# Performance work log

Hardware: AMD Instinct MI355X
Metric: run time of the kernel (lower is better)

The kernel has to match this reference:

```python
import jax, jax.numpy as jnp
import numpy as np

L, H, C, HS, V, BS = 4, 8, 512, 64, 32000, 2048  # layers, heads, n_embd, head_size, vocab, block_size
B, T = 2, 2048


def _ln(x, g, b, eps=1e-5):
    m = jnp.mean(x, axis=-1, keepdims=True)
    v = jnp.var(x, axis=-1, keepdims=True)
    return (x - m) * jax.lax.rsqrt(v + eps) * g + b


def setup_inputs() -> dict:
    key = jax.random.key(0)
    ks = jax.random.split(key, 12)
    s = 0.02
    f = jnp.float32
    return {
        "idx": jax.random.randint(ks[0], (B, T), 0, V),
        "tok_emb": jax.random.normal(ks[1], (V, C), f) * s,
        "pos_emb": jax.random.normal(ks[2], (BS, C), f) * s,
        "ln1_g": jnp.ones((L, C), f), "ln1_b": jnp.zeros((L, C), f),
        "wq": jax.random.normal(ks[3], (L, H, C, HS), f) * s,
        "wk": jax.random.normal(ks[4], (L, H, C, HS), f) * s,
        "wv": jax.random.normal(ks[5], (L, H, C, HS), f) * s,
        "proj_w": jax.random.normal(ks[6], (L, C, C), f) * s,
        "proj_b": jnp.zeros((L, C), f),
        "ln2_g": jnp.ones((L, C), f), "ln2_b": jnp.zeros((L, C), f),
        "ff_w1": jax.random.normal(ks[7], (L, C, 4 * C), f) * s,
        "ff_b1": jnp.zeros((L, 4 * C), f),
        "ff_w2": jax.random.normal(ks[8], (L, 4 * C, C), f) * s,
        "ff_b2": jnp.zeros((L, C), f),
        "ffln_g": jnp.ones((L, C), f), "ffln_b": jnp.zeros((L, C), f),
        "lm_w": jax.random.normal(ks[9], (C, V), f) * s,
        "lm_b": jnp.zeros((V,), f),
    }


def reference(idx, tok_emb, pos_emb, ln1_g, ln1_b, wq, wk, wv, proj_w, proj_b,
              ln2_g, ln2_b, ff_w1, ff_b1, ff_w2, ff_b2, ffln_g, ffln_b, lm_w, lm_b):
    Tn = idx.shape[1]
    x = tok_emb[idx] + pos_emb[:Tn]  # [B,T,C]
    causal = jnp.tril(jnp.ones((Tn, Tn), bool))
    for l in range(L):
        h = _ln(x, ln1_g[l], ln1_b[l])
        q = jnp.einsum('btc,hcd->bhtd', h, wq[l])
        k = jnp.einsum('btc,hcd->bhtd', h, wk[l])
        v = jnp.einsum('btc,hcd->bhtd', h, wv[l])
        # NOTE: original module does NOT scale by 1/sqrt(head_size)
        wei = jnp.einsum('bhtd,bhsd->bhts', q, k)
        wei = jnp.where(causal, wei, -jnp.inf)
        wei = jax.nn.softmax(wei, axis=-1)
        att = jnp.einsum('bhts,bhsd->bhtd', wei, v)  # [B,H,T,HS]
        att = att.transpose(0, 2, 1, 3).reshape(x.shape[0], Tn, C)
        x = x + att @ proj_w[l].T + proj_b[l]
        h2 = _ln(x, ln2_g[l], ln2_b[l])
        ff = jax.nn.relu(h2 @ ff_w1[l] + ff_b1[l]) @ ff_w2[l] + ff_b2[l]
        ff = _ln(ff, ffln_g[l], ffln_b[l])  # FeedForward has trailing LayerNorm
        x = x + ff
    logits = x @ lm_w + lm_b  # [B,T,V]
    return logits
```

## Files before the change

kernel.cpp:

```cpp
#include <hip/hip_runtime.h>
#include <math.h>

#define NLAYER 4
#define NH     8
#define CDIM   512
#define HS     64
#define VOCAB  32000
#define BB     2
#define TT     2048
#define MROWS  (BB*TT)
#define QKVW   (3*CDIM)
#define NHEADS (BB*NH)
#define ASPLIT 4

typedef __attribute__((ext_vector_type(8))) short bf16x8;
typedef __attribute__((ext_vector_type(4))) float f32x4;

__device__ __forceinline__ unsigned short f2bf(float f) {
    unsigned int u = __float_as_uint(f);
    u += 0x7FFF + ((u >> 16) & 1);
    return (unsigned short)(u >> 16);
}

#define GLOAD16(g, l) __builtin_amdgcn_global_load_lds( \
    (const __attribute__((address_space(1))) void*)(g), \
    (__attribute__((address_space(3))) void*)(l), 16, 0, 0)

#define SWZ(row, chunk) (((row)*64) + ((((chunk) ^ ((row)&7)))*8))

template<int FLAGS, bool OUTBF, bool MSWIZ>
__global__ __launch_bounds__(256) void mfma_gemm(
    const unsigned short* __restrict__ A, int lda,
    const unsigned short* __restrict__ Bt, int ldb,
    const float* __restrict__ bias,
    void* __restrict__ Cout, int ldc,
    const float* __restrict__ resid,
    int K)
{
    __shared__ unsigned short As[2][128*64];
    __shared__ unsigned short Bs[2][128*64];
    const int tid = threadIdx.x;
    const int w = tid >> 6, l = tid & 63;
    const int wr = w >> 1, wc = w & 1;
    long m0, n0;
    if (MSWIZ) {
        const int mt = gridDim.x;
        const int flat = blockIdx.y * mt + blockIdx.x;
        const int cpx = (mt * gridDim.y) >> 3;
        const int swz = (flat & 7) * cpx + (flat >> 3);
        m0 = (long)(swz % mt) * 128;
        n0 = (long)(swz / mt) * 128;
    } else {
        m0 = (long)blockIdx.y * 128;
        n0 = (long)blockIdx.x * 128;
    }
    const int srow = l >> 3;
    const int scol = ((l & 7) ^ (srow & 7)) << 3;
    const unsigned short* Ab = A + m0*lda;
    const unsigned short* Bb = Bt + n0*ldb;
    const int fr = l & 15;
    const int g  = l >> 4;

    f32x4 acc[4][4];
    #pragma unroll
    for (int m = 0; m < 4; m++)
        #pragma unroll
        for (int n = 0; n < 4; n++) acc[m][n] = (f32x4)0.0f;

    auto stage = [&](int k0, int buf) {
        #pragma unroll
        for (int i = 0; i < 4; i++) {
            int seg = w*4 + i;
            GLOAD16(Ab + (long)(seg*8 + srow)*lda + k0 + scol, &As[buf][seg*512]);
            GLOAD16(Bb + (long)(seg*8 + srow)*ldb + k0 + scol, &Bs[buf][seg*512]);
        }
    };

    const int nk = K >> 6;
    stage(0, 0);
    for (int ks = 0; ks < nk; ks++) {
        const int buf = ks & 1;
        __syncthreads();
        if (ks + 1 < nk) stage((ks+1) << 6, buf ^ 1);
        #pragma unroll
        for (int kk = 0; kk < 2; kk++) {
            bf16x8 af[4], bf[4];
            #pragma unroll
            for (int m = 0; m < 4; m++) {
                int row = wr*64 + m*16 + fr;
                af[m] = *(const bf16x8*)&As[buf][SWZ(row, kk*4 + g)];
            }
            #pragma unroll
            for (int n = 0; n < 4; n++) {
                int row = wc*64 + n*16 + fr;
                bf[n] = *(const bf16x8*)&Bs[buf][SWZ(row, kk*4 + g)];
            }
            #pragma unroll
            for (int m = 0; m < 4; m++)
                #pragma unroll
                for (int n = 0; n < 4; n++)
                    acc[m][n] = __builtin_amdgcn_mfma_f32_16x16x32_bf16(
                        af[m], bf[n], acc[m][n], 0, 0, 0);
        }
    }

    const int rg = g << 2;
    #pragma unroll
    for (int n = 0; n < 4; n++) {
        long gn = n0 + wc*64 + n*16 + fr;
        float bv = (FLAGS & 1) ? bias[gn] : 0.f;
        #pragma unroll
        for (int m = 0; m < 4; m++) {
            #pragma unroll
            for (int r = 0; r < 4; r++) {
                long gm = m0 + wr*64 + m*16 + rg + r;
                float val = acc[m][n][r] + bv;
                if (FLAGS & 2) val = fmaxf(val, 0.f);
                if (FLAGS & 4) val += resid[gm*ldc + gn];
                if (OUTBF) {
                    ((unsigned short*)Cout)[gm*ldc + gn] = f2bf(val);
                } else if (FLAGS & 8) {
                    __builtin_nontemporal_store(val, &((float*)Cout)[gm*ldc + gn]);
                } else {
                    ((float*)Cout)[gm*ldc + gn] = val;
                }
            }
        }
    }
}

__global__ __launch_bounds__(256) void mfma_gemm_qkv(
    const unsigned short* __restrict__ A,
    const unsigned short* __restrict__ Bt,
    unsigned short* __restrict__ qh,
    unsigned short* __restrict__ kh,
    unsigned short* __restrict__ vt)
{
    __shared__ unsigned short As[2][128*64];
    __shared__ unsigned short Bs[2][128*64];
    const int tid = threadIdx.x;
    const int w = tid >> 6, l = tid & 63;
    const int wr = w >> 1, wc = w & 1;
    const long m0 = (long)blockIdx.y * 128;
    const long n0 = (long)blockIdx.x * 128;
    const int srow = l >> 3;
    const int scol = ((l & 7) ^ (srow & 7)) << 3;
    const unsigned short* Ab = A + m0*CDIM;
    const unsigned short* Bb = Bt + n0*CDIM;
    const int fr = l & 15;
    const int g  = l >> 4;

    f32x4 acc[4][4];
    #pragma unroll
    for (int m = 0; m < 4; m++)
        #pragma unroll
        for (int n = 0; n < 4; n++) acc[m][n] = (f32x4)0.0f;

    auto stage = [&](int k0, int buf) {
        #pragma unroll
        for (int i = 0; i < 4; i++) {
            int seg = w*4 + i;
            GLOAD16(Ab + (long)(seg*8 + srow)*CDIM + k0 + scol, &As[buf][seg*512]);
            GLOAD16(Bb + (long)(seg*8 + srow)*CDIM + k0 + scol, &Bs[buf][seg*512]);
        }
    };

    const int nk = CDIM >> 6;
    stage(0, 0);
    for (int ks = 0; ks < nk; ks++) {
        const int buf = ks & 1;
        __syncthreads();
        if (ks + 1 < nk) stage((ks+1) << 6, buf ^ 1);
        #pragma unroll
        for (int kk = 0; kk < 2; kk++) {
            bf16x8 af[4], bf[4];
            #pragma unroll
            for (int m = 0; m < 4; m++) {
                int row = wr*64 + m*16 + fr;
                af[m] = *(const bf16x8*)&As[buf][SWZ(row, kk*4 + g)];
            }
            #pragma unroll
            for (int n = 0; n < 4; n++) {
                int row = wc*64 + n*16 + fr;
                bf[n] = *(const bf16x8*)&Bs[buf][SWZ(row, kk*4 + g)];
            }
            #pragma unroll
            for (int m = 0; m < 4; m++)
                #pragma unroll
                for (int n = 0; n < 4; n++)
                    acc[m][n] = __builtin_amdgcn_mfma_f32_16x16x32_bf16(
                        af[m], bf[n], acc[m][n], 0, 0, 0);
        }
    }

    const int rg = g << 2;
    #pragma unroll
    for (int n = 0; n < 4; n++) {
        int gn = (int)(n0 + wc*64 + n*16 + fr);
        int which = gn >> 9, hh = (gn >> 6) & 7, d = gn & 63;
        #pragma unroll
        for (int m = 0; m < 4; m++) {
            #pragma unroll
            for (int r = 0; r < 4; r++) {
                int gm = (int)(m0 + wr*64 + m*16 + rg + r);
                int b = gm >> 11, t = gm & (TT-1);
                int head = b*NH + hh;
                unsigned short val = f2bf(acc[m][n][r]);
                if (which == 0)      qh[((long)head*TT + t)*HS + d] = val;
                else if (which == 1) kh[((long)head*TT + t)*HS + d] = val;
                else                 vt[((long)head*HS + d)*TT + t] = val;
            }
        }
    }
}

__global__ __launch_bounds__(256) void attn_part(
    const unsigned short* __restrict__ qh,
    const unsigned short* __restrict__ kh,
    const unsigned short* __restrict__ vt,
    float* __restrict__ oP, float* __restrict__ ml)
{
    __shared__ unsigned short Ks[2][64*64];
    __shared__ unsigned short Vts[2][64*64];
    __shared__ unsigned short Ps[4][32*72];
    const int tid = threadIdx.x;
    const int w = tid >> 6, l = tid & 63;
    const int fr = l & 15, g = l >> 4;
    const int head = blockIdx.y;
    const int sp = blockIdx.z;
    const int x = blockIdx.x;
    const int qw = x*128 + w*32;
    const unsigned short* Qb = qh + (long)head*TT*HS;
    const unsigned short* Kb = kh + (long)head*TT*HS;
    const unsigned short* Vb = vt + (long)head*HS*TT;

    bf16x8 aq[2][2];
    #pragma unroll
    for (int mt = 0; mt < 2; mt++)
        #pragma unroll
        for (int ks = 0; ks < 2; ks++)
            aq[mt][ks] = *(const bf16x8*)&Qb[(long)(qw + mt*16 + fr)*HS + ks*32 + g*8];

    f32x4 acc_o[2][4];
    float mrun[2][4], lsum[2][4];
    #pragma unroll
    for (int mt = 0; mt < 2; mt++) {
        #pragma unroll
        for (int r = 0; r < 4; r++) { mrun[mt][r] = -INFINITY; lsum[mt][r] = 0.f; }
        #pragma unroll
        for (int n = 0; n < 4; n++) acc_o[mt][n] = (f32x4)0.0f;
    }

    const int nch = 2*x + 2;
    const int qq = nch >> 2, rr = nch & 3;
    const int cbeg = sp*qq + (sp < rr ? sp : rr);
    const int cend = cbeg + qq + (sp < rr ? 1 : 0);
    const int srow = l >> 3;
    const int scol = ((l & 7) ^ (srow & 7)) << 3;

    auto stage = [&](int c) {
        int buf = c & 1;
        int s0_ = c*64;
        #pragma unroll
        for (int i = 0; i < 2; i++) {
            int rb = i*32 + w*8;
            GLOAD16(Kb + (long)(s0_ + rb + srow)*HS + scol, &Ks[buf][rb*64]);
            GLOAD16(Vb + (long)(rb + srow)*TT + s0_ + scol, &Vts[buf][rb*64]);
        }
    };

    if (cbeg < cend) stage(cbeg);
    for (int c = cbeg; c < cend; c++) {
        const int s0 = c*64;
        const int buf = c & 1;
        __syncthreads();
        if (c + 1 < cend) stage(c+1);
        if (s0 > qw + 31) continue;

        bf16x8 bk[4][2];
        #pragma unroll
        for (int n = 0; n < 4; n++)
            #pragma unroll
            for (int ks = 0; ks < 2; ks++) {
                int row = n*16 + fr;
                bk[n][ks] = *(const bf16x8*)&Ks[buf][SWZ(row, ks*4 + g)];
            }
        f32x4 sc[2][4];
        #pragma unroll
        for (int mt = 0; mt < 2; mt++)
            #pragma unroll
            for (int n = 0; n < 4; n++) sc[mt][n] = (f32x4)0.0f;
        #pragma unroll
        for (int ks = 0; ks < 2; ks++)
            #pragma unroll
            for (int mt = 0; mt < 2; mt++)
                #pragma unroll
                for (int n = 0; n < 4; n++)
                    sc[mt][n] = __builtin_amdgcn_mfma_f32_16x16x32_bf16(
                        aq[mt][ks], bk[n][ks], sc[mt][n], 0, 0, 0);

        #pragma unroll
        for (int mt = 0; mt < 2; mt++) {
            #pragma unroll
            for (int r = 0; r < 4; r++) {
                int q = qw + mt*16 + g*4 + r;
                float rmax = -INFINITY;
                #pragma unroll
                for (int n = 0; n < 4; n++) {
                    float v = sc[mt][n][r];
                    v = (s0 + n*16 + fr <= q) ? v : -INFINITY;
                    sc[mt][n][r] = v;
                    rmax = fmaxf(rmax, v);
                }
                #pragma unroll
                for (int off = 8; off >= 1; off >>= 1)
                    rmax = fmaxf(rmax, __shfl_xor(rmax, off));
                float mnew = fmaxf(mrun[mt][r], rmax);
                float scale = __expf(mrun[mt][r] - mnew);
                float ps = 0.f;
                #pragma unroll
                for (int n = 0; n < 4; n++) {
                    float p = __expf(sc[mt][n][r] - mnew);
                    sc[mt][n][r] = p;
                    ps += p;
                }
                #pragma unroll
                for (int off = 8; off >= 1; off >>= 1)
                    ps += __shfl_xor(ps, off);
                lsum[mt][r] = lsum[mt][r]*scale + ps;
                mrun[mt][r] = mnew;
                #pragma unroll
                for (int n = 0; n < 4; n++) acc_o[mt][n][r] *= scale;
            }
        }

        #pragma unroll
        for (int mt = 0; mt < 2; mt++)
            #pragma unroll
            for (int n = 0; n < 4; n++)
                #pragma unroll
                for (int r = 0; r < 4; r++)
                    Ps[w][(mt*16 + g*4 + r)*72 + n*16 + fr] = f2bf(sc[mt][n][r]);

        bf16x8 ap[2][2], bv[4][2];
        #pragma unroll
        for (int mt = 0; mt < 2; mt++)
            #pragma unroll
            for (int ks = 0; ks < 2; ks++)
                ap[mt][ks] = *(const bf16x8*)&Ps[w][(mt*16 + fr)*72 + ks*32 + g*8];
        #pragma unroll
        for (int n = 0; n < 4; n++)
            #pragma unroll
            for (int ks = 0; ks < 2; ks++) {
                int row = n*16 + fr;
                bv[n][ks] = *(const bf16x8*)&Vts[buf][SWZ(row, ks*4 + g)];
            }
        #pragma unroll
        for (int ks = 0; ks < 2; ks++)
            #pragma unroll
            for (int mt = 0; mt < 2; mt++)
                #pragma unroll
                for (int n = 0; n < 4; n++)
                    acc_o[mt][n] = __builtin_amdgcn_mfma_f32_16x16x32_bf16(
                        ap[mt][ks], bv[n][ks], acc_o[mt][n], 0, 0, 0);
    }

    float* oB = oP + ((long)(head*ASPLIT + sp)*TT)*HS;
    float* mlB = ml + ((long)(head*ASPLIT + sp)*TT)*2;
    #pragma unroll
    for (int mt = 0; mt < 2; mt++) {
        #pragma unroll
        for (int n = 0; n < 4; n++)
            #pragma unroll
            for (int r = 0; r < 4; r++)
                oB[(long)(qw + mt*16 + g*4 + r)*HS + n*16 + fr] = acc_o[mt][n][r];
        if (fr == 0) {
            #pragma unroll
            for (int r = 0; r < 4; r++) {
                int t = qw + mt*16 + g*4 + r;
                mlB[t*2]     = mrun[mt][r];
                mlB[t*2 + 1] = lsum[mt][r];
            }
        }
    }
}

__global__ __launch_bounds__(256) void attn_combine(
    const float* __restrict__ oP, const float* __restrict__ ml,
    unsigned short* __restrict__ att)
{
    const int gid = blockIdx.x*4 + (threadIdx.x >> 6);
    const int lane = threadIdx.x & 63;
    const int head = gid >> 11, t = gid & (TT-1);
    const int b = head >> 3, hh = head & 7;
    float m[ASPLIT], lv[ASPLIT];
    float M = -INFINITY;
    #pragma unroll
    for (int s = 0; s < ASPLIT; s++) {
        long i = (long)(head*ASPLIT + s)*TT + t;
        m[s] = ml[i*2]; lv[s] = ml[i*2+1];
        M = fmaxf(M, m[s]);
    }
    float L = 0.f, v = 0.f;
    #pragma unroll
    for (int s = 0; s < ASPLIT; s++) {
        float e = __expf(m[s] - M);
        L += lv[s]*e;
        v += oP[((long)(head*ASPLIT + s)*TT + t)*HS + lane]*e;
    }
    att[((long)b*TT + t)*CDIM + hh*HS + lane] = f2bf(v / L);
}

__global__ __launch_bounds__(256) void transpose_cast(
    const float* __restrict__ in, unsigned short* __restrict__ out,
    int R, int Cn, long in_z1, long in_z2, long out_z1, long out_z2, int z2n)
{
    const int z = blockIdx.z;
    const int z1 = z / z2n, z2 = z % z2n;
    const float* ip = in + (long)z1*in_z1 + (long)z2*in_z2;
    unsigned short* op = out + (long)z1*out_z1 + (long)z2*out_z2;
    __shared__ float tile[32][33];
    const int tx = threadIdx.x & 31, ty = threadIdx.x >> 5;
    const long r0 = (long)blockIdx.y*32, c0 = (long)blockIdx.x*32;
    #pragma unroll
    for (int i = 0; i < 4; i++)
        tile[ty + i*8][tx] = ip[(r0 + ty + i*8)*Cn + c0 + tx];
    __syncthreads();
    #pragma unroll
    for (int i = 0; i < 4; i++)
        op[(c0 + ty + i*8)*R + r0 + tx] = f2bf(tile[tx][ty + i*8]);
}

__global__ __launch_bounds__(256) void cast_kernel(
    const float* __restrict__ in, unsigned short* __restrict__ out, long n)
{
    long i = ((long)blockIdx.x*256 + threadIdx.x) * 4;
    if (i >= n) return;
    float4 v = *(const float4*)(in + i);
    ushort4 u = make_ushort4(f2bf(v.x), f2bf(v.y), f2bf(v.z), f2bf(v.w));
    *(ushort4*)(out + i) = u;
}

__global__ void embed_kernel(const int* __restrict__ idx,
                             const float* __restrict__ tok,
                             const float* __restrict__ pos,
                             float* __restrict__ x)
{
    const int r = blockIdx.x;
    const int t = r & (TT-1);
    const long tr = idx[r];
    const float* te = tok + tr*CDIM;
    const float* pe = pos + (long)t*CDIM;
    float* xo = x + (long)r*CDIM;
    for (int c = threadIdx.x; c < CDIM; c += blockDim.x)
        xo[c] = te[c] + pe[c];
}

template<int MODE>
__global__ __launch_bounds__(256) void ln_kernel(
    const float* __restrict__ in, const float* __restrict__ g,
    const float* __restrict__ bb, void* __restrict__ outp,
    void* __restrict__ outp2)
{
    const int wave = threadIdx.x >> 6;
    const int lane = threadIdx.x & 63;
    const long r = (long)blockIdx.x*4 + wave;
    const float* xr = in + r*CDIM;
    float vals[8];
    float s = 0.f;
    #pragma unroll
    for (int i = 0; i < 8; i++) { vals[i] = xr[lane + i*64]; s += vals[i]; }
    #pragma unroll
    for (int o = 32; o >= 1; o >>= 1) s += __shfl_xor(s, o);
    const float mean = s * (1.f/CDIM);
    float vs = 0.f;
    #pragma unroll
    for (int i = 0; i < 8; i++) { float d = vals[i]-mean; vs += d*d; }
    #pragma unroll
    for (int o = 32; o >= 1; o >>= 1) vs += __shfl_xor(vs, o);
    const float rstd = rsqrtf(vs*(1.f/CDIM) + 1e-5f);
    #pragma unroll
    for (int i = 0; i < 8; i++) {
        int c = lane + i*64;
        float nv = (vals[i]-mean)*rstd*g[c] + bb[c];
        if (MODE == 1) {
            ((unsigned short*)outp)[r*CDIM + c] = f2bf(nv);
        } else {
            float s2 = ((float*)outp)[r*CDIM + c] + nv;
            ((float*)outp)[r*CDIM + c] = s2;
            if (MODE == 3) ((unsigned short*)outp2)[r*CDIM + c] = f2bf(s2);
        }
    }
}

extern "C" void kernel_launch(void* const* d_in, const int* in_sizes, int n_in,
                              void* d_out, int out_size, void* d_ws, size_t ws_size,
                              hipStream_t stream)
{
    const int*   idx   = (const int*)  d_in[0];
    const float* tok   = (const float*)d_in[1];
    const float* pos   = (const float*)d_in[2];
    const float* ln1g  = (const float*)d_in[3];
    const float* ln1b  = (const float*)d_in[4];
    const float* wq    = (const float*)d_in[5];
    const float* wk    = (const float*)d_in[6];
    const float* wv    = (const float*)d_in[7];
    const float* projw = (const float*)d_in[8];
    const float* projb = (const float*)d_in[9];
    const float* ln2g  = (const float*)d_in[10];
    const float* ln2b  = (const float*)d_in[11];
    const float* ffw1  = (const float*)d_in[12];
    const float* ffb1  = (const float*)d_in[13];
    const float* ffw2  = (const float*)d_in[14];
    const float* ffb2  = (const float*)d_in[15];
    const float* flng  = (const float*)d_in[16];
    const float* flnb  = (const float*)d_in[17];
    const float* lmw   = (const float*)d_in[18];
    const float* lmb   = (const float*)d_in[19];
    float* out = (float*)d_out;

    char* wp = (char*)d_ws;
    float* x  = (float*)wp;           wp += (size_t)MROWS*CDIM*4;
    float* ff = (float*)wp;           wp += (size_t)MROWS*CDIM*4;
    unsigned short* h     = (unsigned short*)wp; wp += (size_t)MROWS*CDIM*2;
    unsigned short* lmt   = (unsigned short*)wp; wp += (size_t)VOCAB*CDIM*2;
    unsigned short* ff1t  = (unsigned short*)wp; wp += (size_t)NLAYER*4*CDIM*CDIM*2;
    unsigned short* ff2t  = (unsigned short*)wp; wp += (size_t)NLAYER*4*CDIM*CDIM*2;
    unsigned short* qkvt  = (unsigned short*)wp; wp += (size_t)NLAYER*QKVW*CDIM*2;
    unsigned short* projc = (unsigned short*)wp; wp += (size_t)NLAYER*CDIM*CDIM*2;
    unsigned short* qh    = (unsigned short*)wp; wp += (size_t)NHEADS*TT*HS*2;
    unsigned short* kh    = (unsigned short*)wp; wp += (size_t)NHEADS*TT*HS*2;
    unsigned short* vt    = (unsigned short*)wp; wp += (size_t)NHEADS*TT*HS*2;

    unsigned short* f1  = (unsigned short*)d_out;
    unsigned short* att = f1 + (size_t)MROWS*4*CDIM;
    float* oP = (float*)(att + (size_t)MROWS*CDIM);
    float* ml = oP + (size_t)NHEADS*ASPLIT*TT*HS;

    transpose_cast<<<dim3(VOCAB/32, CDIM/32, 1), 256, 0, stream>>>(
        lmw, lmt, CDIM, VOCAB, 0, 0, 0, 0, 1);
    transpose_cast<<<dim3(4*CDIM/32, CDIM/32, NLAYER), 256, 0, stream>>>(
        ffw1, ff1t, CDIM, 4*CDIM, (long)CDIM*4*CDIM, 0, (long)4*CDIM*CDIM, 0, 1);
    transpose_cast<<<dim3(CDIM/32, 4*CDIM/32, NLAYER), 256, 0, stream>>>(
        ffw2, ff2t, 4*CDIM, CDIM, (long)4*CDIM*CDIM, 0, (long)CDIM*4*CDIM, 0, 1);
    {
        const size_t QBLK = (size_t)CDIM * CDIM;
        transpose_cast<<<dim3(HS/32, CDIM/32, NLAYER*NH), 256, 0, stream>>>(
            wq, qkvt,            CDIM, HS,
            (long)NH*CDIM*HS, (long)CDIM*HS, (long)QKVW*CDIM, (long)HS*CDIM, NH);
        transpose_cast<<<dim3(HS/32, CDIM/32, NLAYER*NH), 256, 0, stream>>>(
            wk, qkvt + QBLK,     CDIM, HS,
            (long)NH*CDIM*HS, (long)CDIM*HS, (long)QKVW*CDIM, (long)HS*CDIM, NH);
        transpose_cast<<<dim3(HS/32, CDIM/32, NLAYER*NH), 256, 0, stream>>>(
            wv, qkvt + 2*QBLK,   CDIM, HS,
            (long)NH*CDIM*HS, (long)CDIM*HS, (long)QKVW*CDIM, (long)HS*CDIM, NH);
    }
    cast_kernel<<<(NLAYER*CDIM*CDIM/4 + 255)/256, 256, 0, stream>>>(
        projw, projc, (long)NLAYER*CDIM*CDIM);

    embed_kernel<<<MROWS, 256, 0, stream>>>(idx, tok, pos, x);

    for (int l = 0; l < NLAYER; l++) {
        const unsigned short* qkvt_l = qkvt + (size_t)l*QKVW*CDIM;
        const unsigned short* projc_l = projc + (size_t)l*CDIM*CDIM;
        const unsigned short* ff1t_l = ff1t + (size_t)l*4*CDIM*CDIM;
        const unsigned short* ff2t_l = ff2t + (size_t)l*4*CDIM*CDIM;

        ln_kernel<1><<<MROWS/4, 256, 0, stream>>>(x, ln1g + l*CDIM, ln1b + l*CDIM, h, nullptr);

        mfma_gemm_qkv<<<dim3(QKVW/128, MROWS/128), 256, 0, stream>>>(
            h, qkvt_l, qh, kh, vt);

        attn_part<<<dim3(TT/128, NHEADS, ASPLIT), 256, 0, stream>>>(qh, kh, vt, oP, ml);
        attn_combine<<<dim3(NHEADS*TT/4), 256, 0, stream>>>(oP, ml, att);

        mfma_gemm<5,false,false><<<dim3(CDIM/128, MROWS/128), 256, 0, stream>>>(
            att, CDIM, projc_l, CDIM, projb + l*CDIM, x, CDIM, x, CDIM);

        ln_kernel<1><<<MROWS/4, 256, 0, stream>>>(x, ln2g + l*CDIM, ln2b + l*CDIM, h, nullptr);

        mfma_gemm<3,true,false><<<dim3(4*CDIM/128, MROWS/128), 256, 0, stream>>>(
            h, CDIM, ff1t_l, CDIM, ffb1 + (size_t)l*4*CDIM, f1, 4*CDIM, nullptr, CDIM);

        mfma_gemm<1,false,false><<<dim3(CDIM/128, MROWS/128), 256, 0, stream>>>(
            f1, 4*CDIM, ff2t_l, 4*CDIM, ffb2 + l*CDIM, ff, CDIM, nullptr, 4*CDIM);

        if (l == NLAYER-1)
            ln_kernel<3><<<MROWS/4, 256, 0, stream>>>(ff, flng + l*CDIM, flnb + l*CDIM, x, h);
        else
            ln_kernel<2><<<MROWS/4, 256, 0, stream>>>(ff, flng + l*CDIM, flnb + l*CDIM, x, nullptr);
    }

    mfma_gemm<9,false,true><<<dim3(MROWS/128, VOCAB/128), 256, 0, stream>>>(
        h, CDIM, lmt, CDIM, lmb, out, VOCAB, nullptr, CDIM);
}
```

Before: 975.6 us.

## Split-K the proj and FF2 GEMMs and halve attention split factor

The two narrow-output GEMMs (proj and FF2, N=512 over 4096 rows) launch only 128 tiles each, which underfills the GPU. They now run as split-K partial GEMMs (2-way and 4-way) writing fp32 partials, followed by a reduce kernel that adds the bias and the optional residual. Separately, the attention KV split drops from 4 to 2, which shrinks the partial output buffers and the combine work. The trade-off is extra fp32 partial traffic and an extra launch per GEMM, plus less attention parallelism.

```diff
diff --git a/kernel.cpp b/kernel.cpp
--- a/kernel.cpp
+++ b/kernel.cpp
@@ -11,7 +11,7 @@
 #define MROWS  (BB*TT)
 #define QKVW   (3*CDIM)
 #define NHEADS (BB*NH)
-#define ASPLIT 4
+#define ASPLIT 2
 
 typedef __attribute__((ext_vector_type(8))) short bf16x8;
 typedef __attribute__((ext_vector_type(4))) float f32x4;
@@ -129,6 +129,105 @@
     }
 }
 
+__global__ __launch_bounds__(256) void mfma_gemm_pk(
+    const unsigned short* __restrict__ A, int lda,
+    const unsigned short* __restrict__ Bt, int ldb,
+    float* __restrict__ part, int ldc, long zstride,
+    int Kc)
+{
+    __shared__ unsigned short As[2][128*64];
+    __shared__ unsigned short Bs[2][128*64];
+    const int tid = threadIdx.x;
+    const int w = tid >> 6, l = tid & 63;
+    const int wr = w >> 1, wc = w & 1;
+    const long m0 = (long)blockIdx.y * 128;
+    const long n0 = (long)blockIdx.x * 128;
+    const int z = blockIdx.z;
+    const int srow = l >> 3;
+    const int scol = ((l & 7) ^ (srow & 7)) << 3;
+    const unsigned short* Ab = A + m0*lda + (long)z*Kc;
+    const unsigned short* Bb = Bt + n0*ldb + (long)z*Kc;
+    float* Cb = part + (long)z*zstride;
+    const int fr = l & 15;
+    const int g  = l >> 4;
+
+    f32x4 acc[4][4];
+    #pragma unroll
+    for (int m = 0; m < 4; m++)
+        #pragma unroll
+        for (int n = 0; n < 4; n++) acc[m][n] = (f32x4)0.0f;
+
+    auto stage = [&](int k0, int buf) {
+        #pragma unroll
+        for (int i = 0; i < 4; i++) {
+            int seg = w*4 + i;
+            GLOAD16(Ab + (long)(seg*8 + srow)*lda + k0 + scol, &As[buf][seg*512]);
+            GLOAD16(Bb + (long)(seg*8 + srow)*ldb + k0 + scol, &Bs[buf][seg*512]);
+        }
+    };
+
+    const int nk = Kc >> 6;
+    stage(0, 0);
+    for (int ks = 0; ks < nk; ks++) {
+        const int buf = ks & 1;
+        __syncthreads();
+        if (ks + 1 < nk) stage((ks+1) << 6, buf ^ 1);
+        #pragma unroll
+        for (int kk = 0; kk < 2; kk++) {
+            bf16x8 af[4], bf[4];
+            #pragma unroll
+            for (int m = 0; m < 4; m++) {
+                int row = wr*64 + m*16 + fr;
+                af[m] = *(const bf16x8*)&As[buf][SWZ(row, kk*4 + g)];
+            }
+            #pragma unroll
+            for (int n = 0; n < 4; n++) {
+                int row = wc*64 + n*16 + fr;
+                bf[n] = *(const bf16x8*)&Bs[buf][SWZ(row, kk*4 + g)];
+            }
+            #pragma unroll
+            for (int m = 0; m < 4; m++)
+                #pragma unroll
+                for (int n = 0; n < 4; n++)
+                    acc[m][n] = __builtin_amdgcn_mfma_f32_16x16x32_bf16(
+                        af[m], bf[n], acc[m][n], 0, 0, 0);
+        }
+    }
+
+    const int rg = g << 2;
+    #pragma unroll
+    for (int n = 0; n < 4; n++) {
+        long gn = n0 + wc*64 + n*16 + fr;
+        #pragma unroll
+        for (int m = 0; m < 4; m++)
+            #pragma unroll
+            for (int r = 0; r < 4; r++) {
+                long gm = m0 + wr*64 + m*16 + rg + r;
+                Cb[gm*ldc + gn] = acc[m][n][r];
+            }
+    }
+}
+
+template<int NS, int RESID>
+__global__ __launch_bounds__(256) void reduce_add(
+    const float* __restrict__ part, const float* __restrict__ bias,
+    float* __restrict__ out)
+{
+    const long i4 = ((long)blockIdx.x*256 + threadIdx.x) * 4;
+    float4 s = *(const float4*)(bias + (i4 & (CDIM-1)));
+    #pragma unroll
+    for (int z = 0; z < NS; z++) {
+        float4 p = *(const float4*)(part + (long)z*MROWS*CDIM + i4);
+        s.x += p.x; s.y += p.y; s.z += p.z; s.w += p.w;
+    }
+    float4* o = (float4*)(out + i4);
+    if (RESID) {
+        float4 old = *o;
+        s.x += old.x; s.y += old.y; s.z += old.z; s.w += old.w;
+    }
+    *o = s;
+}
+
 __global__ __launch_bounds__(256) void mfma_gemm_qkv(
     const unsigned short* __restrict__ A,
     const unsigned short* __restrict__ Bt,
@@ -252,7 +351,7 @@
     }
 
     const int nch = 2*x + 2;
-    const int qq = nch >> 2, rr = nch & 3;
+    const int qq = nch / ASPLIT, rr = nch % ASPLIT;
     const int cbeg = sp*qq + (sp < rr ? sp : rr);
     const int cend = cbeg + qq + (sp < rr ? 1 : 0);
     const int srow = l >> 3;
@@ -536,6 +635,8 @@
     unsigned short* att = f1 + (size_t)MROWS*4*CDIM;
     float* oP = (float*)(att + (size_t)MROWS*CDIM);
     float* ml = oP + (size_t)NHEADS*ASPLIT*TT*HS;
+    float* pP = ml + (size_t)NHEADS*ASPLIT*TT*2;
+    float* fP = pP + (size_t)2*MROWS*CDIM;
 
     transpose_cast<<<dim3(VOCAB/32, CDIM/32, 1), 256, 0, stream>>>(
         lmw, lmt, CDIM, VOCAB, 0, 0, 0, 0, 1);
@@ -560,6 +661,8 @@
 
     embed_kernel<<<MROWS, 256, 0, stream>>>(idx, tok, pos, x);
 
+    const int RBLK = (MROWS*CDIM/4) / 256;
+
     for (int l = 0; l < NLAYER; l++) {
         const unsigned short* qkvt_l = qkvt + (size_t)l*QKVW*CDIM;
         const unsigned short* projc_l = projc + (size_t)l*CDIM*CDIM;
@@ -574,16 +677,18 @@
         attn_part<<<dim3(TT/128, NHEADS, ASPLIT), 256, 0, stream>>>(qh, kh, vt, oP, ml);
         attn_combine<<<dim3(NHEADS*TT/4), 256, 0, stream>>>(oP, ml, att);
 
-        mfma_gemm<5,false,false><<<dim3(CDIM/128, MROWS/128), 256, 0, stream>>>(
-            att, CDIM, projc_l, CDIM, projb + l*CDIM, x, CDIM, x, CDIM);
+        mfma_gemm_pk<<<dim3(CDIM/128, MROWS/128, 2), 256, 0, stream>>>(
+            att, CDIM, projc_l, CDIM, pP, CDIM, (long)MROWS*CDIM, 256);
+        reduce_add<2,1><<<RBLK, 256, 0, stream>>>(pP, projb + l*CDIM, x);
 
         ln_kernel<1><<<MROWS/4, 256, 0, stream>>>(x, ln2g + l*CDIM, ln2b + l*CDIM, h, nullptr);
 
         mfma_gemm<3,true,false><<<dim3(4*CDIM/128, MROWS/128), 256, 0, stream>>>(
             h, CDIM, ff1t_l, CDIM, ffb1 + (size_t)l*4*CDIM, f1, 4*CDIM, nullptr, CDIM);
 
-        mfma_gemm<1,false,false><<<dim3(CDIM/128, MROWS/128), 256, 0, stream>>>(
-            f1, 4*CDIM, ff2t_l, 4*CDIM, ffb2 + l*CDIM, ff, CDIM, nullptr, 4*CDIM);
+        mfma_gemm_pk<<<dim3(CDIM/128, MROWS/128, 4), 256, 0, stream>>>(
+            f1, 4*CDIM, ff2t_l, 4*CDIM, fP, CDIM, (long)MROWS*CDIM, 512);
+        reduce_add<4,0><<<RBLK, 256, 0, stream>>>(fP, ffb2 + l*CDIM, ff);
 
         if (l == NLAYER-1)
             ln_kernel<3><<<MROWS/4, 256, 0, stream>>>(ff, flng + l*CDIM, flnb + l*CDIM, x, h);
```

New measurement: 1.004 ms. 2.9% more time.
